# Performance work log

Hardware: AMD Instinct MI355X
Metric: run time of the kernel (lower is better)

Reference implementation:

```python
import jax, jax.numpy as jnp
import numpy as np

HIDDEN = 256
HEADS = 8
HEAD_DIM = HIDDEN // HEADS
NUM_RBF = 32
CUTOFF = 8.0
K_PTS = 4096   # total points (32 molecules x 128)
N_ATOMS = 2048 # total atoms  (32 molecules x 64)
B_MOL = 32


def setup_inputs() -> dict:
    key = jax.random.key(0)
    ks = jax.random.split(key, 12)
    s = 0.02
    return {
        "h_point": jax.random.normal(ks[0], (K_PTS, HIDDEN), jnp.float32),
        "h_atom": jax.random.normal(ks[1], (N_ATOMS, HIDDEN), jnp.float32),
        "pos_point": jax.random.uniform(ks[2], (K_PTS, 3), jnp.float32) * 10.0,
        "pos_atom": jax.random.uniform(ks[3], (N_ATOMS, 3), jnp.float32) * 10.0,
        "Wq": jax.random.normal(ks[4], (HIDDEN, HIDDEN), jnp.float32) * s,
        "bq": jnp.zeros((HIDDEN,), jnp.float32),
        "Wk": jax.random.normal(ks[5], (HIDDEN, HIDDEN), jnp.float32) * s,
        "bk": jnp.zeros((HIDDEN,), jnp.float32),
        "Wv": jax.random.normal(ks[6], (HIDDEN, HIDDEN), jnp.float32) * s,
        "bv": jnp.zeros((HIDDEN,), jnp.float32),
        "Wo": jax.random.normal(ks[7], (HIDDEN, HIDDEN), jnp.float32) * s,
        "bo": jnp.zeros((HIDDEN,), jnp.float32),
        "W_rbf": jax.random.normal(ks[8], (NUM_RBF, HEADS), jnp.float32) * 0.1,
        "b_rbf": jnp.zeros((HEADS,), jnp.float32),
        "centers": jnp.linspace(0.0, CUTOFF, NUM_RBF, dtype=jnp.float32),
        "gamma": jnp.ones((HIDDEN,), jnp.float32),
        "beta": jnp.zeros((HIDDEN,), jnp.float32),
        "point_batch": jnp.repeat(jnp.arange(B_MOL), K_PTS // B_MOL),
        "atom_batch": jnp.repeat(jnp.arange(B_MOL), N_ATOMS // B_MOL),
    }


def reference(h_point, h_atom, pos_point, pos_atom,
              Wq, bq, Wk, bk, Wv, bv, Wo, bo,
              W_rbf, b_rbf, centers, gamma, beta,
              point_batch, atom_batch):
    H, D = HEADS, HEAD_DIM
    Kp = h_point.shape[0]
    Na = h_atom.shape[0]
    scale = D ** -0.5
    width = (CUTOFF / NUM_RBF) ** 2

    q = (h_point @ Wq + bq).reshape(Kp, H, D)
    k = (h_atom @ Wk + bk).reshape(Na, H, D)
    v = (h_atom @ Wv + bv).reshape(Na, H, D)

    # pairwise distances [Kp, Na]
    d2 = jnp.sum((pos_point[:, None, :] - pos_atom[None, :, :]) ** 2, axis=-1)
    dist = jnp.sqrt(jnp.maximum(d2, 0.0))

    # RBF distance bias -> [H, Kp, Na]
    rbf = jnp.exp(-((dist[..., None] - centers) ** 2) / width)  # [Kp, Na, NUM_RBF]
    bias = (rbf @ W_rbf + b_rbf).transpose(2, 0, 1)

    scores = jnp.einsum('khd,nhd->hkn', q, k) * scale + bias
    # ragged structure: point j only attends to atoms in the same molecule
    mask = point_batch[:, None] == atom_batch[None, :]  # [Kp, Na]
    scores = jnp.where(mask[None], scores, -1e30)
    attn = jax.nn.softmax(scores, axis=-1)

    agg = jnp.einsum('hkn,nhd->khd', attn, v).reshape(Kp, H * D)
    agg = agg @ Wo + bo

    x = h_point + agg
    mean = jnp.mean(x, axis=-1, keepdims=True)
    var = jnp.mean((x - mean) ** 2, axis=-1, keepdims=True)
    return (x - mean) * jax.lax.rsqrt(var + 1e-5) * gamma + beta
```

## Files before the change

### kernel.cpp

```cpp
#include <hip/hip_runtime.h>
#include <hip/hip_bf16.h>

#define HIDDEN 256
#define HEADS 8
#define HEAD_DIM 32
#define NUM_RBF 32
#define K_PTS 4096
#define N_ATOMS 2048
#define B_MOL 32
#define ATOMS_PER_MOL (N_ATOMS / B_MOL)

typedef __attribute__((ext_vector_type(8))) short bf16x8;
typedef __attribute__((ext_vector_type(4))) float f32x4;

__global__ __launch_bounds__(256) void prepW_kernel(
    const float* __restrict__ Wq, const float* __restrict__ Wk,
    const float* __restrict__ Wv, const float* __restrict__ Wo,
    __hip_bfloat16* __restrict__ WqT, __hip_bfloat16* __restrict__ WkT,
    __hip_bfloat16* __restrict__ WvT, __hip_bfloat16* __restrict__ WoT) {
    __shared__ float tile[32][33];
    const int t = blockIdx.x, tid = threadIdx.x;
    const int matId = t >> 6, tileId = t & 63;
    const int tr = (tileId >> 3) * 32, tc = (tileId & 7) * 32;
    const float* __restrict__ Ws = (matId == 0) ? Wq : (matId == 1) ? Wk : (matId == 2) ? Wv : Wo;
    __hip_bfloat16* __restrict__ Wd = (matId == 0) ? WqT : (matId == 1) ? WkT : (matId == 2) ? WvT : WoT;

    const int r = tid >> 3, cq = (tid & 7) * 4;
    const float4 in = *(const float4*)&Ws[(size_t)(tr + r) * HIDDEN + tc + cq];
    tile[r][cq + 0] = in.x; tile[r][cq + 1] = in.y;
    tile[r][cq + 2] = in.z; tile[r][cq + 3] = in.w;
    __syncthreads();
    __hip_bfloat16 o[4];
    o[0] = __float2bfloat16(tile[cq + 0][r]);
    o[1] = __float2bfloat16(tile[cq + 1][r]);
    o[2] = __float2bfloat16(tile[cq + 2][r]);
    o[3] = __float2bfloat16(tile[cq + 3][r]);
    *(uint2*)(Wd + (size_t)(tc + r) * HIDDEN + tr + cq) = *(const uint2*)o;
}

__device__ __forceinline__ bf16x8 cvt8(const float* p) {
    const float4 lo = *(const float4*)p;
    const float4 hi = *(const float4*)(p + 4);
    __hip_bfloat16 t[8];
    t[0] = __float2bfloat16(lo.x); t[1] = __float2bfloat16(lo.y);
    t[2] = __float2bfloat16(lo.z); t[3] = __float2bfloat16(lo.w);
    t[4] = __float2bfloat16(hi.x); t[5] = __float2bfloat16(hi.y);
    t[6] = __float2bfloat16(hi.z); t[7] = __float2bfloat16(hi.w);
    return *(const bf16x8*)t;
}

__global__ __launch_bounds__(256) void qkv2_kernel(
    const float* __restrict__ hp, const float* __restrict__ ha,
    const __hip_bfloat16* __restrict__ WqT, const float* __restrict__ bq, float* __restrict__ q_ws,
    const __hip_bfloat16* __restrict__ WkT, const float* __restrict__ bk, float* __restrict__ k_ws,
    const __hip_bfloat16* __restrict__ WvT, const float* __restrict__ bv, float* __restrict__ v_ws) {
    const bool isQ = (blockIdx.x < 256);
    const float* __restrict__ A = isQ ? hp : ha;
    const __hip_bfloat16* __restrict__ W0T = isQ ? WqT : WkT;
    const float* __restrict__ b0 = isQ ? bq : bk;
    float* __restrict__ C0 = isQ ? q_ws : k_ws;
    const int r0 = (isQ ? blockIdx.x : blockIdx.x - 256) * 16;

    const int wave = threadIdx.x >> 6, lane = threadIdx.x & 63;
    const int c0 = wave * 64;
    const int lrow = lane & 15, kgrp = lane >> 4;

    bf16x8 af[8];
    const float* Arow = A + (size_t)(r0 + lrow) * HIDDEN + kgrp * 8;
#pragma unroll
    for (int ks = 0; ks < 8; ++ks)
        af[ks] = cvt8(Arow + ks * 32);

    f32x4 acc0[4], acc1[4];
#pragma unroll
    for (int cc = 0; cc < 4; ++cc) {
        acc0[cc] = (f32x4){0.f, 0.f, 0.f, 0.f};
        acc1[cc] = (f32x4){0.f, 0.f, 0.f, 0.f};
    }

#pragma unroll
    for (int cc = 0; cc < 4; ++cc) {
        const short* W0r = (const short*)W0T + (size_t)(c0 + cc * 16 + lrow) * HIDDEN + kgrp * 8;
#pragma unroll
        for (int ks = 0; ks < 8; ++ks)
            acc0[cc] = __builtin_amdgcn_mfma_f32_16x16x32_bf16(
                af[ks], *(const bf16x8*)(W0r + ks * 32), acc0[cc], 0, 0, 0);
        if (!isQ) {
            const short* W1r = (const short*)WvT + (size_t)(c0 + cc * 16 + lrow) * HIDDEN + kgrp * 8;
#pragma unroll
            for (int ks = 0; ks < 8; ++ks)
                acc1[cc] = __builtin_amdgcn_mfma_f32_16x16x32_bf16(
                    af[ks], *(const bf16x8*)(W1r + ks * 32), acc1[cc], 0, 0, 0);
        }
    }

    const int colb = lane & 15;
    const int rowb = (lane >> 4) * 4;
#pragma unroll
    for (int cc = 0; cc < 4; ++cc) {
        const int cgl = c0 + cc * 16 + colb;
        const float bias0 = b0[cgl];
#pragma unroll
        for (int rg = 0; rg < 4; ++rg)
            C0[(size_t)(r0 + rowb + rg) * HIDDEN + cgl] = acc0[cc][rg] + bias0;
        if (!isQ) {
            const float bias1 = bv[cgl];
#pragma unroll
            for (int rg = 0; rg < 4; ++rg)
                v_ws[(size_t)(r0 + rowb + rg) * HIDDEN + cgl] = acc1[cc][rg] + bias1;
        }
    }
}

#define AGG_PAD (HIDDEN + 16)
#define X_PAD (HIDDEN + 4)

__global__ __launch_bounds__(256) void attn_oln_kernel(
    const float* __restrict__ q, const float* __restrict__ kmat,
    const float* __restrict__ vmat,
    const float* __restrict__ pos_point, const float* __restrict__ pos_atom,
    const float* __restrict__ W_rbf, const float* __restrict__ b_rbf,
    const float* __restrict__ centers,
    const int* __restrict__ point_batch, const int* __restrict__ atom_batch,
    const __hip_bfloat16* __restrict__ WoT, const float* __restrict__ bo,
    const float* __restrict__ h_point,
    const float* __restrict__ gamma, const float* __restrict__ beta,
    float* __restrict__ out) {
    __shared__ float q_lds[8][HIDDEN];
    __shared__ float wrbf_lds[NUM_RBF][HEADS];
    __shared__ float cent_lds[NUM_RBF];
    __shared__ float brbf_lds[HEADS];
    __shared__ float w_lds[4][2][HEADS][72];
    __shared__ __hip_bfloat16 agg_lds[8][AGG_PAD];
    __shared__ float x_lds[8][X_PAD];
    __shared__ float red_s[8][4];
    __shared__ float red_q[8][4];

    const int tid = threadIdx.x, wave = tid >> 6, lane = tid & 63;
    const int j0 = blockIdx.x * 8;

    {
        const float4* s4 = (const float4*)(q + (size_t)j0 * HIDDEN);
        float4* d4 = (float4*)&q_lds[0][0];
        d4[tid] = s4[tid];
        d4[tid + 256] = s4[tid + 256];
    }
    if (tid < NUM_RBF * HEADS) ((float*)wrbf_lds)[tid] = W_rbf[tid];
    if (tid < NUM_RBF) cent_lds[tid] = centers[tid];
    if (tid < HEADS) brbf_lds[tid] = b_rbf[tid];
    __syncthreads();

    const int jA = j0 + wave * 2, jB = jA + 1;
    const int m = point_batch[jA];
    const int n = m * ATOMS_PER_MOL + lane;
    const bool valid = (atom_batch[n] == m);

    const float ax = pos_atom[n * 3 + 0], ay = pos_atom[n * 3 + 1], az = pos_atom[n * 3 + 2];
    const float dxA = pos_point[jA * 3 + 0] - ax;
    const float dyA = pos_point[jA * 3 + 1] - ay;
    const float dzA = pos_point[jA * 3 + 2] - az;
    const float dxB = pos_point[jB * 3 + 0] - ax;
    const float dyB = pos_point[jB * 3 + 1] - ay;
    const float dzB = pos_point[jB * 3 + 2] - az;
    const float distA = sqrtf(fmaxf(dxA * dxA + dyA * dyA + dzA * dzA, 0.0f));
    const float distB = sqrtf(fmaxf(dxB * dxB + dyB * dyB + dzB * dzB, 0.0f));

    float biasA[HEADS], biasB[HEADS];
#pragma unroll
    for (int h = 0; h < HEADS; ++h) { biasA[h] = brbf_lds[h]; biasB[h] = brbf_lds[h]; }
#pragma unroll
    for (int r = 0; r < NUM_RBF; ++r) {
        const float c = cent_lds[r];
        const float ddA = distA - c, ddB = distB - c;
        const float eA = __expf(-16.0f * ddA * ddA);
        const float eB = __expf(-16.0f * ddB * ddB);
#pragma unroll
        for (int h = 0; h < HEADS; ++h) {
            const float wr = wrbf_lds[r][h];
            biasA[h] += eA * wr;
            biasB[h] += eB * wr;
        }
    }

    const float scale = 0.17677669529663687f;
    const float* krow = kmat + (size_t)n * HIDDEN;

#pragma unroll
    for (int h = 0; h < HEADS; ++h) {
        const float4* k4 = (const float4*)(krow + h * HEAD_DIM);
        const float4* qA4 = (const float4*)(&q_lds[wave * 2 + 0][h * HEAD_DIM]);
        const float4* qB4 = (const float4*)(&q_lds[wave * 2 + 1][h * HEAD_DIM]);
        float dotA = 0.f, dotB = 0.f;
#pragma unroll
        for (int i = 0; i < HEAD_DIM / 4; ++i) {
            const float4 kv = k4[i];
            const float4 qa = qA4[i];
            const float4 qb = qB4[i];
            dotA += kv.x * qa.x + kv.y * qa.y + kv.z * qa.z + kv.w * qa.w;
            dotB += kv.x * qb.x + kv.y * qb.y + kv.z * qb.z + kv.w * qb.w;
        }
        float sA = valid ? (dotA * scale + biasA[h]) : -1e30f;
        float sB = valid ? (dotB * scale + biasB[h]) : -1e30f;

        float mA = sA, mB = sB;
#pragma unroll
        for (int off = 32; off > 0; off >>= 1) {
            mA = fmaxf(mA, __shfl_xor(mA, off));
            mB = fmaxf(mB, __shfl_xor(mB, off));
        }
        const float eA = __expf(sA - mA);
        const float eB = __expf(sB - mB);
        float ssA = eA, ssB = eB;
#pragma unroll
        for (int off = 32; off > 0; off >>= 1) {
            ssA += __shfl_xor(ssA, off);
            ssB += __shfl_xor(ssB, off);
        }
        w_lds[wave][0][h][lane] = eA / ssA;
        w_lds[wave][1][h][lane] = eB / ssB;
    }

    const int c4 = lane * 4;
    const int hh = lane >> 3;
    {
        const float* wA = &w_lds[wave][0][hh][0];
        const float* wB = &w_lds[wave][1][hh][0];
        const float* vbase = vmat + (size_t)(m * ATOMS_PER_MOL) * HIDDEN + c4;
        float4 accA = {0.f, 0.f, 0.f, 0.f};
        float4 accB = {0.f, 0.f, 0.f, 0.f};
#pragma unroll
        for (int a4 = 0; a4 < ATOMS_PER_MOL / 4; ++a4) {
            const float4 wa = *(const float4*)&wA[a4 * 4];
            const float4 wb = *(const float4*)&wB[a4 * 4];
            const float4 v0 = *(const float4*)(vbase + (size_t)(a4 * 4 + 0) * HIDDEN);
            const float4 v1 = *(const float4*)(vbase + (size_t)(a4 * 4 + 1) * HIDDEN);
            const float4 v2 = *(const float4*)(vbase + (size_t)(a4 * 4 + 2) * HIDDEN);
            const float4 v3 = *(const float4*)(vbase + (size_t)(a4 * 4 + 3) * HIDDEN);
            accA.x += wa.x * v0.x + wa.y * v1.x + wa.z * v2.x + wa.w * v3.x;
            accA.y += wa.x * v0.y + wa.y * v1.y + wa.z * v2.y + wa.w * v3.y;
            accA.z += wa.x * v0.z + wa.y * v1.z + wa.z * v2.z + wa.w * v3.z;
            accA.w += wa.x * v0.w + wa.y * v1.w + wa.z * v2.w + wa.w * v3.w;
            accB.x += wb.x * v0.x + wb.y * v1.x + wb.z * v2.x + wb.w * v3.x;
            accB.y += wb.x * v0.y + wb.y * v1.y + wb.z * v2.y + wb.w * v3.y;
            accB.z += wb.x * v0.z + wb.y * v1.z + wb.z * v2.z + wb.w * v3.z;
            accB.w += wb.x * v0.w + wb.y * v1.w + wb.z * v2.w + wb.w * v3.w;
        }
        __hip_bfloat16 oA[4], oB[4];
        oA[0] = __float2bfloat16(accA.x); oA[1] = __float2bfloat16(accA.y);
        oA[2] = __float2bfloat16(accA.z); oA[3] = __float2bfloat16(accA.w);
        oB[0] = __float2bfloat16(accB.x); oB[1] = __float2bfloat16(accB.y);
        oB[2] = __float2bfloat16(accB.z); oB[3] = __float2bfloat16(accB.w);
        *(uint2*)(&agg_lds[wave * 2 + 0][c4]) = *(const uint2*)oA;
        *(uint2*)(&agg_lds[wave * 2 + 1][c4]) = *(const uint2*)oB;
    }
    __syncthreads();

    const int c0 = wave * 64;
    const int lrow = lane & 15, kgrp = lane >> 4;
    bf16x8 af[8];
    const bf16x8 zf = {0, 0, 0, 0, 0, 0, 0, 0};
#pragma unroll
    for (int ks = 0; ks < 8; ++ks)
        af[ks] = (lrow < 8) ? *(const bf16x8*)(&agg_lds[lrow & 7][kgrp * 8 + ks * 32]) : zf;

    f32x4 acc[4];
#pragma unroll
    for (int cc = 0; cc < 4; ++cc) acc[cc] = (f32x4){0.f, 0.f, 0.f, 0.f};
#pragma unroll
    for (int cc = 0; cc < 4; ++cc) {
        const short* Wr = (const short*)WoT + (size_t)(c0 + cc * 16 + lrow) * HIDDEN + kgrp * 8;
#pragma unroll
        for (int ks = 0; ks < 8; ++ks)
            acc[cc] = __builtin_amdgcn_mfma_f32_16x16x32_bf16(
                af[ks], *(const bf16x8*)(Wr + ks * 32), acc[cc], 0, 0, 0);
    }

    const int colb = lane & 15;
    const int rowb = (lane >> 4) * 4;
#pragma unroll
    for (int cc = 0; cc < 4; ++cc) {
        const int cgl = c0 + cc * 16 + colb;
        const float bias = bo[cgl];
#pragma unroll
        for (int rg = 0; rg < 4; ++rg) {
            const int rl = rowb + rg;
            if (rl < 8)
                x_lds[rl][cgl] = acc[cc][rg] + bias + h_point[(size_t)(j0 + rl) * HIDDEN + cgl];
        }
    }
    __syncthreads();

    const int c = tid;
    const int ln = c & 63, wv = c >> 6;
    float xv[8];
#pragma unroll
    for (int r = 0; r < 8; ++r) {
        xv[r] = x_lds[r][c];
        float s = xv[r], qq = xv[r] * xv[r];
#pragma unroll
        for (int off = 32; off > 0; off >>= 1) {
            s += __shfl_xor(s, off);
            qq += __shfl_xor(qq, off);
        }
        if (ln == 0) { red_s[r][wv] = s; red_q[r][wv] = qq; }
    }
    __syncthreads();

    const float gc = gamma[c], bc = beta[c];
#pragma unroll
    for (int r = 0; r < 8; ++r) {
        const float mean = (red_s[r][0] + red_s[r][1] + red_s[r][2] + red_s[r][3]) * (1.0f / HIDDEN);
        const float ex2  = (red_q[r][0] + red_q[r][1] + red_q[r][2] + red_q[r][3]) * (1.0f / HIDDEN);
        const float var = ex2 - mean * mean;
        out[(size_t)(j0 + r) * HIDDEN + c] = (xv[r] - mean) * rsqrtf(var + 1e-5f) * gc + bc;
    }
}

extern "C" void kernel_launch(void* const* d_in, const int* in_sizes, int n_in,
                              void* d_out, int out_size, void* d_ws, size_t ws_size,
                              hipStream_t stream) {
    const float* h_point   = (const float*)d_in[0];
    const float* h_atom    = (const float*)d_in[1];
    const float* pos_point = (const float*)d_in[2];
    const float* pos_atom  = (const float*)d_in[3];
    const float* Wq        = (const float*)d_in[4];
    const float* bq        = (const float*)d_in[5];
    const float* Wk        = (const float*)d_in[6];
    const float* bk        = (const float*)d_in[7];
    const float* Wv        = (const float*)d_in[8];
    const float* bv        = (const float*)d_in[9];
    const float* Wo        = (const float*)d_in[10];
    const float* bo        = (const float*)d_in[11];
    const float* W_rbf     = (const float*)d_in[12];
    const float* b_rbf     = (const float*)d_in[13];
    const float* centers   = (const float*)d_in[14];
    const float* gamma     = (const float*)d_in[15];
    const float* beta      = (const float*)d_in[16];
    const int*   point_batch = (const int*)d_in[17];
    const int*   atom_batch  = (const int*)d_in[18];
    float* out = (float*)d_out;

    float* q_ws = (float*)d_ws;
    float* k_ws = q_ws + (size_t)K_PTS * HIDDEN;
    float* v_ws = k_ws + (size_t)N_ATOMS * HIDDEN;
    __hip_bfloat16* WqT = (__hip_bfloat16*)(v_ws + (size_t)N_ATOMS * HIDDEN);
    __hip_bfloat16* WkT = WqT + HIDDEN * HIDDEN;
    __hip_bfloat16* WvT = WkT + HIDDEN * HIDDEN;
    __hip_bfloat16* WoT = WvT + HIDDEN * HIDDEN;

    prepW_kernel<<<256, 256, 0, stream>>>(Wq, Wk, Wv, Wo, WqT, WkT, WvT, WoT);

    qkv2_kernel<<<384, 256, 0, stream>>>(h_point, h_atom,
                                         WqT, bq, q_ws,
                                         WkT, bk, k_ws,
                                         WvT, bv, v_ws);

    attn_oln_kernel<<<K_PTS / 8, 256, 0, stream>>>(q_ws, k_ws, v_ws,
                                                   pos_point, pos_atom,
                                                   W_rbf, b_rbf, centers,
                                                   point_batch, atom_batch,
                                                   WoT, bo, h_point, gamma, beta,
                                                   out);
}
```

Before: 146.7 us.

## Store K/V as bf16 and split attention work across waves by head

The Q/K/V projection kernel now writes K and V as bf16 instead of fp32, which halves the traffic for the attention kernel's K/V reads. The attention kernel is reorganized so each block handles 4 points instead of 8. Each wave now owns 2 heads across all 4 points rather than 2 points across all heads, which cuts per-thread RBF and exp work and lets K rows be reused across points. The grid doubles to 1024 blocks for better occupancy, at the cost of scalar 2-byte V loads and reduced precision for K/V.

```diff
diff --git a/kernel.cpp b/kernel.cpp
--- a/kernel.cpp
+++ b/kernel.cpp
@@ -52,13 +52,12 @@
 __global__ __launch_bounds__(256) void qkv2_kernel(
     const float* __restrict__ hp, const float* __restrict__ ha,
     const __hip_bfloat16* __restrict__ WqT, const float* __restrict__ bq, float* __restrict__ q_ws,
-    const __hip_bfloat16* __restrict__ WkT, const float* __restrict__ bk, float* __restrict__ k_ws,
-    const __hip_bfloat16* __restrict__ WvT, const float* __restrict__ bv, float* __restrict__ v_ws) {
+    const __hip_bfloat16* __restrict__ WkT, const float* __restrict__ bk, __hip_bfloat16* __restrict__ k_bf,
+    const __hip_bfloat16* __restrict__ WvT, const float* __restrict__ bv, __hip_bfloat16* __restrict__ v_bf) {
     const bool isQ = (blockIdx.x < 256);
     const float* __restrict__ A = isQ ? hp : ha;
     const __hip_bfloat16* __restrict__ W0T = isQ ? WqT : WkT;
     const float* __restrict__ b0 = isQ ? bq : bk;
-    float* __restrict__ C0 = isQ ? q_ws : k_ws;
     const int r0 = (isQ ? blockIdx.x : blockIdx.x - 256) * 16;
 
     const int wave = threadIdx.x >> 6, lane = threadIdx.x & 63;
@@ -100,24 +99,32 @@
     for (int cc = 0; cc < 4; ++cc) {
         const int cgl = c0 + cc * 16 + colb;
         const float bias0 = b0[cgl];
-#pragma unroll
-        for (int rg = 0; rg < 4; ++rg)
-            C0[(size_t)(r0 + rowb + rg) * HIDDEN + cgl] = acc0[cc][rg] + bias0;
-        if (!isQ) {
+        if (isQ) {
+#pragma unroll
+            for (int rg = 0; rg < 4; ++rg)
+                q_ws[(size_t)(r0 + rowb + rg) * HIDDEN + cgl] = acc0[cc][rg] + bias0;
+        } else {
             const float bias1 = bv[cgl];
 #pragma unroll
-            for (int rg = 0; rg < 4; ++rg)
-                v_ws[(size_t)(r0 + rowb + rg) * HIDDEN + cgl] = acc1[cc][rg] + bias1;
-        }
-    }
-}
-
+            for (int rg = 0; rg < 4; ++rg) {
+                k_bf[(size_t)(r0 + rowb + rg) * HIDDEN + cgl] = __float2bfloat16(acc0[cc][rg] + bias0);
+                v_bf[(size_t)(r0 + rowb + rg) * HIDDEN + cgl] = __float2bfloat16(acc1[cc][rg] + bias1);
+            }
+        }
+    }
+}
+
+#define W_PAD 72
 #define AGG_PAD (HIDDEN + 16)
-#define X_PAD (HIDDEN + 4)
-
-__global__ __launch_bounds__(256) void attn_oln_kernel(
-    const float* __restrict__ q, const float* __restrict__ kmat,
-    const float* __restrict__ vmat,
+
+__device__ __forceinline__ void unpack2(unsigned u, float& lo, float& hi) {
+    lo = __uint_as_float(u << 16);
+    hi = __uint_as_float(u & 0xffff0000u);
+}
+
+__global__ __launch_bounds__(256) void attn_oln4_kernel(
+    const float* __restrict__ q, const __hip_bfloat16* __restrict__ kmat,
+    const __hip_bfloat16* __restrict__ vmat,
     const float* __restrict__ pos_point, const float* __restrict__ pos_atom,
     const float* __restrict__ W_rbf, const float* __restrict__ b_rbf,
     const float* __restrict__ centers,
@@ -126,132 +133,131 @@
     const float* __restrict__ h_point,
     const float* __restrict__ gamma, const float* __restrict__ beta,
     float* __restrict__ out) {
-    __shared__ float q_lds[8][HIDDEN];
+    __shared__ float q_lds[4][260];
     __shared__ float wrbf_lds[NUM_RBF][HEADS];
     __shared__ float cent_lds[NUM_RBF];
     __shared__ float brbf_lds[HEADS];
-    __shared__ float w_lds[4][2][HEADS][72];
-    __shared__ __hip_bfloat16 agg_lds[8][AGG_PAD];
-    __shared__ float x_lds[8][X_PAD];
-    __shared__ float red_s[8][4];
-    __shared__ float red_q[8][4];
+    __shared__ float p_lds[4][2][4][W_PAD];
+    __shared__ __hip_bfloat16 agg_lds[4][AGG_PAD];
+    __shared__ float x_lds[4][260];
+    __shared__ float red_s[4][4];
+    __shared__ float red_q[4][4];
 
     const int tid = threadIdx.x, wave = tid >> 6, lane = tid & 63;
-    const int j0 = blockIdx.x * 8;
+    const int j0 = blockIdx.x * 4;
 
     {
-        const float4* s4 = (const float4*)(q + (size_t)j0 * HIDDEN);
-        float4* d4 = (float4*)&q_lds[0][0];
-        d4[tid] = s4[tid];
-        d4[tid + 256] = s4[tid + 256];
-    }
-    if (tid < NUM_RBF * HEADS) ((float*)wrbf_lds)[tid] = W_rbf[tid];
+        const int row = tid >> 6, c4 = (tid & 63) * 4;
+        *(float4*)&q_lds[row][c4] = *(const float4*)(q + (size_t)(j0 + row) * HIDDEN + c4);
+    }
+    ((float*)wrbf_lds)[tid & 255] = W_rbf[tid & 255];
     if (tid < NUM_RBF) cent_lds[tid] = centers[tid];
     if (tid < HEADS) brbf_lds[tid] = b_rbf[tid];
     __syncthreads();
 
-    const int jA = j0 + wave * 2, jB = jA + 1;
-    const int m = point_batch[jA];
+    const int m = point_batch[j0];
     const int n = m * ATOMS_PER_MOL + lane;
     const bool valid = (atom_batch[n] == m);
+    const int h0 = wave * 2;
 
     const float ax = pos_atom[n * 3 + 0], ay = pos_atom[n * 3 + 1], az = pos_atom[n * 3 + 2];
-    const float dxA = pos_point[jA * 3 + 0] - ax;
-    const float dyA = pos_point[jA * 3 + 1] - ay;
-    const float dzA = pos_point[jA * 3 + 2] - az;
-    const float dxB = pos_point[jB * 3 + 0] - ax;
-    const float dyB = pos_point[jB * 3 + 1] - ay;
-    const float dzB = pos_point[jB * 3 + 2] - az;
-    const float distA = sqrtf(fmaxf(dxA * dxA + dyA * dyA + dzA * dzA, 0.0f));
-    const float distB = sqrtf(fmaxf(dxB * dxB + dyB * dyB + dzB * dzB, 0.0f));
-
-    float biasA[HEADS], biasB[HEADS];
-#pragma unroll
-    for (int h = 0; h < HEADS; ++h) { biasA[h] = brbf_lds[h]; biasB[h] = brbf_lds[h]; }
+    float dist[4];
+#pragma unroll
+    for (int p = 0; p < 4; ++p) {
+        const float dx = pos_point[(j0 + p) * 3 + 0] - ax;
+        const float dy = pos_point[(j0 + p) * 3 + 1] - ay;
+        const float dz = pos_point[(j0 + p) * 3 + 2] - az;
+        dist[p] = sqrtf(fmaxf(dx * dx + dy * dy + dz * dz, 0.0f));
+    }
+
+    float bias[4][2];
+#pragma unroll
+    for (int p = 0; p < 4; ++p) {
+        bias[p][0] = brbf_lds[h0];
+        bias[p][1] = brbf_lds[h0 + 1];
+    }
 #pragma unroll
     for (int r = 0; r < NUM_RBF; ++r) {
-        const float c = cent_lds[r];
-        const float ddA = distA - c, ddB = distB - c;
-        const float eA = __expf(-16.0f * ddA * ddA);
-        const float eB = __expf(-16.0f * ddB * ddB);
-#pragma unroll
-        for (int h = 0; h < HEADS; ++h) {
-            const float wr = wrbf_lds[r][h];
-            biasA[h] += eA * wr;
-            biasB[h] += eB * wr;
+        const float cr = cent_lds[r];
+        const float w0 = wrbf_lds[r][h0], w1 = wrbf_lds[r][h0 + 1];
+#pragma unroll
+        for (int p = 0; p < 4; ++p) {
+            const float dd = dist[p] - cr;
+            const float e = __expf(-16.0f * dd * dd);
+            bias[p][0] += e * w0;
+            bias[p][1] += e * w1;
         }
     }
 
     const float scale = 0.17677669529663687f;
-    const float* krow = kmat + (size_t)n * HIDDEN;
-
-#pragma unroll
-    for (int h = 0; h < HEADS; ++h) {
-        const float4* k4 = (const float4*)(krow + h * HEAD_DIM);
-        const float4* qA4 = (const float4*)(&q_lds[wave * 2 + 0][h * HEAD_DIM]);
-        const float4* qB4 = (const float4*)(&q_lds[wave * 2 + 1][h * HEAD_DIM]);
-        float dotA = 0.f, dotB = 0.f;
-#pragma unroll
-        for (int i = 0; i < HEAD_DIM / 4; ++i) {
-            const float4 kv = k4[i];
-            const float4 qa = qA4[i];
-            const float4 qb = qB4[i];
-            dotA += kv.x * qa.x + kv.y * qa.y + kv.z * qa.z + kv.w * qa.w;
-            dotB += kv.x * qb.x + kv.y * qb.y + kv.z * qb.z + kv.w * qb.w;
-        }
-        float sA = valid ? (dotA * scale + biasA[h]) : -1e30f;
-        float sB = valid ? (dotB * scale + biasB[h]) : -1e30f;
-
-        float mA = sA, mB = sB;
-#pragma unroll
-        for (int off = 32; off > 0; off >>= 1) {
-            mA = fmaxf(mA, __shfl_xor(mA, off));
-            mB = fmaxf(mB, __shfl_xor(mB, off));
-        }
-        const float eA = __expf(sA - mA);
-        const float eB = __expf(sB - mB);
-        float ssA = eA, ssB = eB;
-#pragma unroll
-        for (int off = 32; off > 0; off >>= 1) {
-            ssA += __shfl_xor(ssA, off);
-            ssB += __shfl_xor(ssB, off);
-        }
-        w_lds[wave][0][h][lane] = eA / ssA;
-        w_lds[wave][1][h][lane] = eB / ssB;
-    }
-
-    const int c4 = lane * 4;
-    const int hh = lane >> 3;
+
+#pragma unroll
+    for (int hl = 0; hl < 2; ++hl) {
+        const unsigned* kr = (const unsigned*)((const unsigned short*)kmat +
+                             (size_t)n * HIDDEN + (h0 + hl) * HEAD_DIM);
+        float kf[32];
+#pragma unroll
+        for (int i = 0; i < 16; ++i)
+            unpack2(kr[i], kf[2 * i], kf[2 * i + 1]);
+
+        float dot[4] = {0.f, 0.f, 0.f, 0.f};
+#pragma unroll
+        for (int i = 0; i < 8; ++i) {
+            const int qo = (h0 + hl) * HEAD_DIM + i * 4;
+            const float4 q0 = *(const float4*)&q_lds[0][qo];
+            const float4 q1 = *(const float4*)&q_lds[1][qo];
+            const float4 q2 = *(const float4*)&q_lds[2][qo];
+            const float4 q3 = *(const float4*)&q_lds[3][qo];
+            dot[0] += q0.x * kf[4*i] + q0.y * kf[4*i+1] + q0.z * kf[4*i+2] + q0.w * kf[4*i+3];
+            dot[1] += q1.x * kf[4*i] + q1.y * kf[4*i+1] + q1.z * kf[4*i+2] + q1.w * kf[4*i+3];
+            dot[2] += q2.x * kf[4*i] + q2.y * kf[4*i+1] + q2.z * kf[4*i+2] + q2.w * kf[4*i+3];
+            dot[3] += q3.x * kf[4*i] + q3.y * kf[4*i+1] + q3.z * kf[4*i+2] + q3.w * kf[4*i+3];
+        }
+#pragma unroll
+        for (int p = 0; p < 4; ++p) {
+            float score = valid ? (dot[p] * scale + bias[p][hl]) : -1e30f;
+            float mx = score;
+#pragma unroll
+            for (int off = 32; off > 0; off >>= 1)
+                mx = fmaxf(mx, __shfl_xor(mx, off));
+            const float e = __expf(score - mx);
+            float ss = e;
+#pragma unroll
+            for (int off = 32; off > 0; off >>= 1)
+                ss += __shfl_xor(ss, off);
+            p_lds[wave][hl][p][lane] = e / ss;
+        }
+    }
+
     {
-        const float* wA = &w_lds[wave][0][hh][0];
-        const float* wB = &w_lds[wave][1][hh][0];
-        const float* vbase = vmat + (size_t)(m * ATOMS_PER_MOL) * HIDDEN + c4;
-        float4 accA = {0.f, 0.f, 0.f, 0.f};
-        float4 accB = {0.f, 0.f, 0.f, 0.f};
-#pragma unroll
-        for (int a4 = 0; a4 < ATOMS_PER_MOL / 4; ++a4) {
-            const float4 wa = *(const float4*)&wA[a4 * 4];
-            const float4 wb = *(const float4*)&wB[a4 * 4];
-            const float4 v0 = *(const float4*)(vbase + (size_t)(a4 * 4 + 0) * HIDDEN);
-            const float4 v1 = *(const float4*)(vbase + (size_t)(a4 * 4 + 1) * HIDDEN);
-            const float4 v2 = *(const float4*)(vbase + (size_t)(a4 * 4 + 2) * HIDDEN);
-            const float4 v3 = *(const float4*)(vbase + (size_t)(a4 * 4 + 3) * HIDDEN);
-            accA.x += wa.x * v0.x + wa.y * v1.x + wa.z * v2.x + wa.w * v3.x;
-            accA.y += wa.x * v0.y + wa.y * v1.y + wa.z * v2.y + wa.w * v3.y;
-            accA.z += wa.x * v0.z + wa.y * v1.z + wa.z * v2.z + wa.w * v3.z;
-            accA.w += wa.x * v0.w + wa.y * v1.w + wa.z * v2.w + wa.w * v3.w;
-            accB.x += wb.x * v0.x + wb.y * v1.x + wb.z * v2.x + wb.w * v3.x;
-            accB.y += wb.x * v0.y + wb.y * v1.y + wb.z * v2.y + wb.w * v3.y;
-            accB.z += wb.x * v0.z + wb.y * v1.z + wb.z * v2.z + wb.w * v3.z;
-            accB.w += wb.x * v0.w + wb.y * v1.w + wb.z * v2.w + wb.w * v3.w;
-        }
-        __hip_bfloat16 oA[4], oB[4];
-        oA[0] = __float2bfloat16(accA.x); oA[1] = __float2bfloat16(accA.y);
-        oA[2] = __float2bfloat16(accA.z); oA[3] = __float2bfloat16(accA.w);
-        oB[0] = __float2bfloat16(accB.x); oB[1] = __float2bfloat16(accB.y);
-        oB[2] = __float2bfloat16(accB.z); oB[3] = __float2bfloat16(accB.w);
-        *(uint2*)(&agg_lds[wave * 2 + 0][c4]) = *(const uint2*)oA;
-        *(uint2*)(&agg_lds[wave * 2 + 1][c4]) = *(const uint2*)oB;
+        const int c = tid;
+        const int hl2 = (lane >> 5) & 1;
+        const unsigned short* vbase = (const unsigned short*)vmat +
+                                      (size_t)(m * ATOMS_PER_MOL) * HIDDEN + c;
+        float acc[4] = {0.f, 0.f, 0.f, 0.f};
+#pragma unroll
+        for (int ag = 0; ag < ATOMS_PER_MOL / 4; ++ag) {
+            const float4 p0 = *(const float4*)&p_lds[wave][hl2][0][ag * 4];
+            const float4 p1 = *(const float4*)&p_lds[wave][hl2][1][ag * 4];
+            const float4 p2 = *(const float4*)&p_lds[wave][hl2][2][ag * 4];
+            const float4 p3 = *(const float4*)&p_lds[wave][hl2][3][ag * 4];
+            const float* pp0 = (const float*)&p0;
+            const float* pp1 = (const float*)&p1;
+            const float* pp2 = (const float*)&p2;
+            const float* pp3 = (const float*)&p3;
+#pragma unroll
+            for (int i = 0; i < 4; ++i) {
+                const int a = ag * 4 + i;
+                const float v = __uint_as_float(((unsigned)vbase[(size_t)a * HIDDEN]) << 16);
+                acc[0] += pp0[i] * v;
+                acc[1] += pp1[i] * v;
+                acc[2] += pp2[i] * v;
+                acc[3] += pp3[i] * v;
+            }
+        }
+#pragma unroll
+        for (int p = 0; p < 4; ++p)
+            agg_lds[p][c] = __float2bfloat16(acc[p]);
     }
     __syncthreads();
 
@@ -261,7 +267,7 @@
     const bf16x8 zf = {0, 0, 0, 0, 0, 0, 0, 0};
 #pragma unroll
     for (int ks = 0; ks < 8; ++ks)
-        af[ks] = (lrow < 8) ? *(const bf16x8*)(&agg_lds[lrow & 7][kgrp * 8 + ks * 32]) : zf;
+        af[ks] = (lrow < 4) ? *(const bf16x8*)(&agg_lds[lrow & 3][kgrp * 8 + ks * 32]) : zf;
 
     f32x4 acc[4];
 #pragma unroll
@@ -280,21 +286,21 @@
 #pragma unroll
     for (int cc = 0; cc < 4; ++cc) {
         const int cgl = c0 + cc * 16 + colb;
-        const float bias = bo[cgl];
+        const float bias_o = bo[cgl];
 #pragma unroll
         for (int rg = 0; rg < 4; ++rg) {
             const int rl = rowb + rg;
-            if (rl < 8)
-                x_lds[rl][cgl] = acc[cc][rg] + bias + h_point[(size_t)(j0 + rl) * HIDDEN + cgl];
+            if (rl < 4)
+                x_lds[rl][cgl] = acc[cc][rg] + bias_o + h_point[(size_t)(j0 + rl) * HIDDEN + cgl];
         }
     }
     __syncthreads();
 
     const int c = tid;
     const int ln = c & 63, wv = c >> 6;
-    float xv[8];
-#pragma unroll
-    for (int r = 0; r < 8; ++r) {
+    float xv[4];
+#pragma unroll
+    for (int r = 0; r < 4; ++r) {
         xv[r] = x_lds[r][c];
         float s = xv[r], qq = xv[r] * xv[r];
 #pragma unroll
@@ -308,7 +314,7 @@
 
     const float gc = gamma[c], bc = beta[c];
 #pragma unroll
-    for (int r = 0; r < 8; ++r) {
+    for (int r = 0; r < 4; ++r) {
         const float mean = (red_s[r][0] + red_s[r][1] + red_s[r][2] + red_s[r][3]) * (1.0f / HIDDEN);
         const float ex2  = (red_q[r][0] + red_q[r][1] + red_q[r][2] + red_q[r][3]) * (1.0f / HIDDEN);
         const float var = ex2 - mean * mean;
@@ -341,9 +347,9 @@
     float* out = (float*)d_out;
 
     float* q_ws = (float*)d_ws;
-    float* k_ws = q_ws + (size_t)K_PTS * HIDDEN;
-    float* v_ws = k_ws + (size_t)N_ATOMS * HIDDEN;
-    __hip_bfloat16* WqT = (__hip_bfloat16*)(v_ws + (size_t)N_ATOMS * HIDDEN);
+    __hip_bfloat16* k_bf = (__hip_bfloat16*)(q_ws + (size_t)K_PTS * HIDDEN);
+    __hip_bfloat16* v_bf = k_bf + (size_t)N_ATOMS * HIDDEN;
+    __hip_bfloat16* WqT = v_bf + (size_t)N_ATOMS * HIDDEN;
     __hip_bfloat16* WkT = WqT + HIDDEN * HIDDEN;
     __hip_bfloat16* WvT = WkT + HIDDEN * HIDDEN;
     __hip_bfloat16* WoT = WvT + HIDDEN * HIDDEN;
@@ -352,13 +358,13 @@
 
     qkv2_kernel<<<384, 256, 0, stream>>>(h_point, h_atom,
                                          WqT, bq, q_ws,
-                                         WkT, bk, k_ws,
-                                         WvT, bv, v_ws);
-
-    attn_oln_kernel<<<K_PTS / 8, 256, 0, stream>>>(q_ws, k_ws, v_ws,
-                                                   pos_point, pos_atom,
-                                                   W_rbf, b_rbf, centers,
-                                                   point_batch, atom_batch,
-                                                   WoT, bo, h_point, gamma, beta,
-                                                   out);
-}
+                                         WkT, bk, k_bf,
+                                         WvT, bv, v_bf);
+
+    attn_oln4_kernel<<<K_PTS / 4, 256, 0, stream>>>(q_ws, k_bf, v_bf,
+                                                    pos_point, pos_atom,
+                                                    W_rbf, b_rbf, centers,
+                                                    point_batch, atom_batch,
+                                                    WoT, bo, h_point, gamma, beta,
+                                                    out);
+}
```

After: 180.8 us. 23.2% more time.

## Compute attention scores and PV product with bf16 MFMA, store Q/K/V in bf16

Applied to the files above, without the earlier changes.

The QKV projection kernel now writes Q and K as bf16 and V transposed as bf16. The attention kernel swaps the scalar fp32 dot products and the weighted V sum for 16x16x32 bf16 MFMA instructions. The RBF bias is staged in LDS per head and atom, and the softmax runs on MFMA accumulator fragments using 16-lane shuffles. This cuts global traffic for Q/K/V and moves the attention arithmetic onto matrix cores, at the cost of lower precision on scores and probabilities and a strided transposed V store.

```diff
diff --git a/kernel.cpp b/kernel.cpp
--- a/kernel.cpp
+++ b/kernel.cpp
@@ -49,16 +49,15 @@
     return *(const bf16x8*)t;
 }
 
-__global__ __launch_bounds__(256) void qkv2_kernel(
+__global__ __launch_bounds__(256) void qkv3_kernel(
     const float* __restrict__ hp, const float* __restrict__ ha,
-    const __hip_bfloat16* __restrict__ WqT, const float* __restrict__ bq, float* __restrict__ q_ws,
-    const __hip_bfloat16* __restrict__ WkT, const float* __restrict__ bk, float* __restrict__ k_ws,
-    const __hip_bfloat16* __restrict__ WvT, const float* __restrict__ bv, float* __restrict__ v_ws) {
+    const __hip_bfloat16* __restrict__ WqT, const float* __restrict__ bq, __hip_bfloat16* __restrict__ qb,
+    const __hip_bfloat16* __restrict__ WkT, const float* __restrict__ bk, __hip_bfloat16* __restrict__ kb,
+    const __hip_bfloat16* __restrict__ WvT, const float* __restrict__ bv, __hip_bfloat16* __restrict__ vt) {
     const bool isQ = (blockIdx.x < 256);
     const float* __restrict__ A = isQ ? hp : ha;
     const __hip_bfloat16* __restrict__ W0T = isQ ? WqT : WkT;
     const float* __restrict__ b0 = isQ ? bq : bk;
-    float* __restrict__ C0 = isQ ? q_ws : k_ws;
     const int r0 = (isQ ? blockIdx.x : blockIdx.x - 256) * 16;
 
     const int wave = threadIdx.x >> 6, lane = threadIdx.x & 63;
@@ -100,24 +99,26 @@
     for (int cc = 0; cc < 4; ++cc) {
         const int cgl = c0 + cc * 16 + colb;
         const float bias0 = b0[cgl];
-#pragma unroll
-        for (int rg = 0; rg < 4; ++rg)
-            C0[(size_t)(r0 + rowb + rg) * HIDDEN + cgl] = acc0[cc][rg] + bias0;
-        if (!isQ) {
+        if (isQ) {
+#pragma unroll
+            for (int rg = 0; rg < 4; ++rg)
+                qb[(size_t)(r0 + rowb + rg) * HIDDEN + cgl] = __float2bfloat16(acc0[cc][rg] + bias0);
+        } else {
             const float bias1 = bv[cgl];
 #pragma unroll
-            for (int rg = 0; rg < 4; ++rg)
-                v_ws[(size_t)(r0 + rowb + rg) * HIDDEN + cgl] = acc1[cc][rg] + bias1;
+            for (int rg = 0; rg < 4; ++rg) {
+                kb[(size_t)(r0 + rowb + rg) * HIDDEN + cgl] = __float2bfloat16(acc0[cc][rg] + bias0);
+                vt[(size_t)cgl * N_ATOMS + (r0 + rowb + rg)] = __float2bfloat16(acc1[cc][rg] + bias1);
+            }
         }
     }
 }
 
 #define AGG_PAD (HIDDEN + 16)
-#define X_PAD (HIDDEN + 4)
-
-__global__ __launch_bounds__(256) void attn_oln_kernel(
-    const float* __restrict__ q, const float* __restrict__ kmat,
-    const float* __restrict__ vmat,
+
+__global__ __launch_bounds__(256) void attn_mfma_kernel(
+    const __hip_bfloat16* __restrict__ qb, const __hip_bfloat16* __restrict__ kb,
+    const __hip_bfloat16* __restrict__ vt,
     const float* __restrict__ pos_point, const float* __restrict__ pos_atom,
     const float* __restrict__ W_rbf, const float* __restrict__ b_rbf,
     const float* __restrict__ centers,
@@ -126,153 +127,159 @@
     const float* __restrict__ h_point,
     const float* __restrict__ gamma, const float* __restrict__ beta,
     float* __restrict__ out) {
-    __shared__ float q_lds[8][HIDDEN];
     __shared__ float wrbf_lds[NUM_RBF][HEADS];
     __shared__ float cent_lds[NUM_RBF];
     __shared__ float brbf_lds[HEADS];
-    __shared__ float w_lds[4][2][HEADS][72];
+    __shared__ float bias_lds[HEADS][ATOMS_PER_MOL + 1][8];
+    __shared__ __hip_bfloat16 p_lds[HEADS][8][72];
     __shared__ __hip_bfloat16 agg_lds[8][AGG_PAD];
-    __shared__ float x_lds[8][X_PAD];
+    __shared__ float x_lds[8][260];
     __shared__ float red_s[8][4];
     __shared__ float red_q[8][4];
 
     const int tid = threadIdx.x, wave = tid >> 6, lane = tid & 63;
     const int j0 = blockIdx.x * 8;
-
-    {
-        const float4* s4 = (const float4*)(q + (size_t)j0 * HIDDEN);
-        float4* d4 = (float4*)&q_lds[0][0];
-        d4[tid] = s4[tid];
-        d4[tid + 256] = s4[tid + 256];
-    }
-    if (tid < NUM_RBF * HEADS) ((float*)wrbf_lds)[tid] = W_rbf[tid];
+    const float scale = 0.17677669529663687f;
+
+    ((float*)wrbf_lds)[tid] = W_rbf[tid];
     if (tid < NUM_RBF) cent_lds[tid] = centers[tid];
     if (tid < HEADS) brbf_lds[tid] = b_rbf[tid];
-    __syncthreads();
-
-    const int jA = j0 + wave * 2, jB = jA + 1;
-    const int m = point_batch[jA];
-    const int n = m * ATOMS_PER_MOL + lane;
-    const bool valid = (atom_batch[n] == m);
-
-    const float ax = pos_atom[n * 3 + 0], ay = pos_atom[n * 3 + 1], az = pos_atom[n * 3 + 2];
-    const float dxA = pos_point[jA * 3 + 0] - ax;
-    const float dyA = pos_point[jA * 3 + 1] - ay;
-    const float dzA = pos_point[jA * 3 + 2] - az;
-    const float dxB = pos_point[jB * 3 + 0] - ax;
-    const float dyB = pos_point[jB * 3 + 1] - ay;
-    const float dzB = pos_point[jB * 3 + 2] - az;
-    const float distA = sqrtf(fmaxf(dxA * dxA + dyA * dyA + dzA * dzA, 0.0f));
-    const float distB = sqrtf(fmaxf(dxB * dxB + dyB * dyB + dzB * dzB, 0.0f));
-
-    float biasA[HEADS], biasB[HEADS];
-#pragma unroll
-    for (int h = 0; h < HEADS; ++h) { biasA[h] = brbf_lds[h]; biasB[h] = brbf_lds[h]; }
-#pragma unroll
-    for (int r = 0; r < NUM_RBF; ++r) {
-        const float c = cent_lds[r];
-        const float ddA = distA - c, ddB = distB - c;
-        const float eA = __expf(-16.0f * ddA * ddA);
-        const float eB = __expf(-16.0f * ddB * ddB);
+    if (tid < 64) {
+        bias_lds[tid >> 3][ATOMS_PER_MOL][tid & 7] = 0.0f;
+    }
+    __syncthreads();
+
+    const int m = point_batch[j0];
+    const int mbase = m * ATOMS_PER_MOL;
+
+    {
+        const int n = mbase + lane;
+        const bool valid = (atom_batch[n] == m);
+        const int jA = j0 + wave * 2, jB = jA + 1;
+
+        const float ax = pos_atom[n * 3 + 0], ay = pos_atom[n * 3 + 1], az = pos_atom[n * 3 + 2];
+        const float dxA = pos_point[jA * 3 + 0] - ax;
+        const float dyA = pos_point[jA * 3 + 1] - ay;
+        const float dzA = pos_point[jA * 3 + 2] - az;
+        const float dxB = pos_point[jB * 3 + 0] - ax;
+        const float dyB = pos_point[jB * 3 + 1] - ay;
+        const float dzB = pos_point[jB * 3 + 2] - az;
+        const float distA = sqrtf(fmaxf(dxA * dxA + dyA * dyA + dzA * dzA, 0.0f));
+        const float distB = sqrtf(fmaxf(dxB * dxB + dyB * dyB + dzB * dzB, 0.0f));
+
+        float biasA[HEADS], biasB[HEADS];
+#pragma unroll
+        for (int h = 0; h < HEADS; ++h) { biasA[h] = brbf_lds[h]; biasB[h] = brbf_lds[h]; }
+#pragma unroll
+        for (int r = 0; r < NUM_RBF; ++r) {
+            const float cr = cent_lds[r];
+            const float ddA = distA - cr, ddB = distB - cr;
+            const float eA = __expf(-16.0f * ddA * ddA);
+            const float eB = __expf(-16.0f * ddB * ddB);
+#pragma unroll
+            for (int h = 0; h < HEADS; ++h) {
+                const float wr = wrbf_lds[r][h];
+                biasA[h] += eA * wr;
+                biasB[h] += eB * wr;
+            }
+        }
 #pragma unroll
         for (int h = 0; h < HEADS; ++h) {
-            const float wr = wrbf_lds[r][h];
-            biasA[h] += eA * wr;
-            biasB[h] += eB * wr;
-        }
-    }
-
-    const float scale = 0.17677669529663687f;
-    const float* krow = kmat + (size_t)n * HIDDEN;
-
-#pragma unroll
-    for (int h = 0; h < HEADS; ++h) {
-        const float4* k4 = (const float4*)(krow + h * HEAD_DIM);
-        const float4* qA4 = (const float4*)(&q_lds[wave * 2 + 0][h * HEAD_DIM]);
-        const float4* qB4 = (const float4*)(&q_lds[wave * 2 + 1][h * HEAD_DIM]);
-        float dotA = 0.f, dotB = 0.f;
-#pragma unroll
-        for (int i = 0; i < HEAD_DIM / 4; ++i) {
-            const float4 kv = k4[i];
-            const float4 qa = qA4[i];
-            const float4 qb = qB4[i];
-            dotA += kv.x * qa.x + kv.y * qa.y + kv.z * qa.z + kv.w * qa.w;
-            dotB += kv.x * qb.x + kv.y * qb.y + kv.z * qb.z + kv.w * qb.w;
-        }
-        float sA = valid ? (dotA * scale + biasA[h]) : -1e30f;
-        float sB = valid ? (dotB * scale + biasB[h]) : -1e30f;
-
-        float mA = sA, mB = sB;
-#pragma unroll
-        for (int off = 32; off > 0; off >>= 1) {
-            mA = fmaxf(mA, __shfl_xor(mA, off));
-            mB = fmaxf(mB, __shfl_xor(mB, off));
-        }
-        const float eA = __expf(sA - mA);
-        const float eB = __expf(sB - mB);
-        float ssA = eA, ssB = eB;
-#pragma unroll
-        for (int off = 32; off > 0; off >>= 1) {
-            ssA += __shfl_xor(ssA, off);
-            ssB += __shfl_xor(ssB, off);
-        }
-        w_lds[wave][0][h][lane] = eA / ssA;
-        w_lds[wave][1][h][lane] = eB / ssB;
-    }
-
-    const int c4 = lane * 4;
-    const int hh = lane >> 3;
-    {
-        const float* wA = &w_lds[wave][0][hh][0];
-        const float* wB = &w_lds[wave][1][hh][0];
-        const float* vbase = vmat + (size_t)(m * ATOMS_PER_MOL) * HIDDEN + c4;
-        float4 accA = {0.f, 0.f, 0.f, 0.f};
-        float4 accB = {0.f, 0.f, 0.f, 0.f};
-#pragma unroll
-        for (int a4 = 0; a4 < ATOMS_PER_MOL / 4; ++a4) {
-            const float4 wa = *(const float4*)&wA[a4 * 4];
-            const float4 wb = *(const float4*)&wB[a4 * 4];
-            const float4 v0 = *(const float4*)(vbase + (size_t)(a4 * 4 + 0) * HIDDEN);
-            const float4 v1 = *(const float4*)(vbase + (size_t)(a4 * 4 + 1) * HIDDEN);
-            const float4 v2 = *(const float4*)(vbase + (size_t)(a4 * 4 + 2) * HIDDEN);
-            const float4 v3 = *(const float4*)(vbase + (size_t)(a4 * 4 + 3) * HIDDEN);
-            accA.x += wa.x * v0.x + wa.y * v1.x + wa.z * v2.x + wa.w * v3.x;
-            accA.y += wa.x * v0.y + wa.y * v1.y + wa.z * v2.y + wa.w * v3.y;
-            accA.z += wa.x * v0.z + wa.y * v1.z + wa.z * v2.z + wa.w * v3.z;
-            accA.w += wa.x * v0.w + wa.y * v1.w + wa.z * v2.w + wa.w * v3.w;
-            accB.x += wb.x * v0.x + wb.y * v1.x + wb.z * v2.x + wb.w * v3.x;
-            accB.y += wb.x * v0.y + wb.y * v1.y + wb.z * v2.y + wb.w * v3.y;
-            accB.z += wb.x * v0.z + wb.y * v1.z + wb.z * v2.z + wb.w * v3.z;
-            accB.w += wb.x * v0.w + wb.y * v1.w + wb.z * v2.w + wb.w * v3.w;
-        }
-        __hip_bfloat16 oA[4], oB[4];
-        oA[0] = __float2bfloat16(accA.x); oA[1] = __float2bfloat16(accA.y);
-        oA[2] = __float2bfloat16(accA.z); oA[3] = __float2bfloat16(accA.w);
-        oB[0] = __float2bfloat16(accB.x); oB[1] = __float2bfloat16(accB.y);
-        oB[2] = __float2bfloat16(accB.z); oB[3] = __float2bfloat16(accB.w);
-        *(uint2*)(&agg_lds[wave * 2 + 0][c4]) = *(const uint2*)oA;
-        *(uint2*)(&agg_lds[wave * 2 + 1][c4]) = *(const uint2*)oB;
+            bias_lds[h][lane][wave * 2 + 0] = valid ? biasA[h] : -1e30f;
+            bias_lds[h][lane][wave * 2 + 1] = valid ? biasB[h] : -1e30f;
+        }
+    }
+    __syncthreads();
+
+    const int c = lane & 15, kgrp = lane >> 4;
+    const int h0 = wave * 2;
+
+#pragma unroll
+    for (int hl = 0; hl < 2; ++hl) {
+        const int h = h0 + hl;
+
+        const bf16x8 aq = *(const bf16x8*)((const short*)qb +
+                          (size_t)(j0 + (c & 7)) * HIDDEN + h * HEAD_DIM + kgrp * 8);
+
+        f32x4 sacc[4];
+#pragma unroll
+        for (int t = 0; t < 4; ++t) {
+            const bf16x8 bk_ = *(const bf16x8*)((const short*)kb +
+                               (size_t)(mbase + c + 16 * t) * HIDDEN + h * HEAD_DIM + kgrp * 8);
+            sacc[t] = __builtin_amdgcn_mfma_f32_16x16x32_bf16(
+                aq, bk_, (f32x4){0.f, 0.f, 0.f, 0.f}, 0, 0, 0);
+        }
+
+        float s[4][4];
+#pragma unroll
+        for (int t = 0; t < 4; ++t) {
+            const f32x4 bv = *(const f32x4*)&bias_lds[h][c + 16 * t][kgrp * 4];
+#pragma unroll
+            for (int r = 0; r < 4; ++r)
+                s[t][r] = sacc[t][r] * scale + bv[r];
+        }
+#pragma unroll
+        for (int r = 0; r < 4; ++r) {
+            float mx = fmaxf(fmaxf(s[0][r], s[1][r]), fmaxf(s[2][r], s[3][r]));
+#pragma unroll
+            for (int off = 1; off <= 8; off <<= 1)
+                mx = fmaxf(mx, __shfl_xor(mx, off));
+            float e0 = __expf(s[0][r] - mx);
+            float e1 = __expf(s[1][r] - mx);
+            float e2 = __expf(s[2][r] - mx);
+            float e3 = __expf(s[3][r] - mx);
+            float ss = e0 + e1 + e2 + e3;
+#pragma unroll
+            for (int off = 1; off <= 8; off <<= 1)
+                ss += __shfl_xor(ss, off);
+            const float inv = 1.0f / ss;
+            if (kgrp < 2) {
+                const int pt = kgrp * 4 + r;
+                p_lds[h][pt][c + 16 * 0] = __float2bfloat16(e0 * inv);
+                p_lds[h][pt][c + 16 * 1] = __float2bfloat16(e1 * inv);
+                p_lds[h][pt][c + 16 * 2] = __float2bfloat16(e2 * inv);
+                p_lds[h][pt][c + 16 * 3] = __float2bfloat16(e3 * inv);
+            }
+        }
+
+#pragma unroll
+        for (int t2 = 0; t2 < 2; ++t2) {
+            f32x4 pacc = (f32x4){0.f, 0.f, 0.f, 0.f};
+#pragma unroll
+            for (int ks = 0; ks < 2; ++ks) {
+                const bf16x8 ap = *(const bf16x8*)&p_lds[h][c & 7][ks * 32 + kgrp * 8];
+                const bf16x8 bvv = *(const bf16x8*)((const short*)vt +
+                                   (size_t)(h * HEAD_DIM + t2 * 16 + c) * N_ATOMS +
+                                   mbase + ks * 32 + kgrp * 8);
+                pacc = __builtin_amdgcn_mfma_f32_16x16x32_bf16(ap, bvv, pacc, 0, 0, 0);
+            }
+            if (kgrp < 2) {
+#pragma unroll
+                for (int r = 0; r < 4; ++r)
+                    agg_lds[kgrp * 4 + r][h * HEAD_DIM + t2 * 16 + c] = __float2bfloat16(pacc[r]);
+            }
+        }
     }
     __syncthreads();
 
     const int c0 = wave * 64;
-    const int lrow = lane & 15, kgrp = lane >> 4;
+    const int lrow = lane & 15, kgrp2 = lane >> 4;
     bf16x8 af[8];
     const bf16x8 zf = {0, 0, 0, 0, 0, 0, 0, 0};
 #pragma unroll
     for (int ks = 0; ks < 8; ++ks)
-        af[ks] = (lrow < 8) ? *(const bf16x8*)(&agg_lds[lrow & 7][kgrp * 8 + ks * 32]) : zf;
-
-    f32x4 acc[4];
-#pragma unroll
-    for (int cc = 0; cc < 4; ++cc) acc[cc] = (f32x4){0.f, 0.f, 0.f, 0.f};
-#pragma unroll
-    for (int cc = 0; cc < 4; ++cc) {
-        const short* Wr = (const short*)WoT + (size_t)(c0 + cc * 16 + lrow) * HIDDEN + kgrp * 8;
+        af[ks] = (lrow < 8) ? *(const bf16x8*)(&agg_lds[lrow & 7][kgrp2 * 8 + ks * 32]) : zf;
+
+    f32x4 oacc[4];
+#pragma unroll
+    for (int cc = 0; cc < 4; ++cc) oacc[cc] = (f32x4){0.f, 0.f, 0.f, 0.f};
+#pragma unroll
+    for (int cc = 0; cc < 4; ++cc) {
+        const short* Wr = (const short*)WoT + (size_t)(c0 + cc * 16 + lrow) * HIDDEN + kgrp2 * 8;
 #pragma unroll
         for (int ks = 0; ks < 8; ++ks)
-            acc[cc] = __builtin_amdgcn_mfma_f32_16x16x32_bf16(
-                af[ks], *(const bf16x8*)(Wr + ks * 32), acc[cc], 0, 0, 0);
+            oacc[cc] = __builtin_amdgcn_mfma_f32_16x16x32_bf16(
+                af[ks], *(const bf16x8*)(Wr + ks * 32), oacc[cc], 0, 0, 0);
     }
 
     const int colb = lane & 15;
@@ -280,22 +287,22 @@
 #pragma unroll
     for (int cc = 0; cc < 4; ++cc) {
         const int cgl = c0 + cc * 16 + colb;
-        const float bias = bo[cgl];
+        const float bias_o = bo[cgl];
 #pragma unroll
         for (int rg = 0; rg < 4; ++rg) {
             const int rl = rowb + rg;
             if (rl < 8)
-                x_lds[rl][cgl] = acc[cc][rg] + bias + h_point[(size_t)(j0 + rl) * HIDDEN + cgl];
-        }
-    }
-    __syncthreads();
-
-    const int c = tid;
-    const int ln = c & 63, wv = c >> 6;
+                x_lds[rl][cgl] = oacc[cc][rg] + bias_o + h_point[(size_t)(j0 + rl) * HIDDEN + cgl];
+        }
+    }
+    __syncthreads();
+
+    const int cc2 = tid;
+    const int ln = cc2 & 63, wv = cc2 >> 6;
     float xv[8];
 #pragma unroll
     for (int r = 0; r < 8; ++r) {
-        xv[r] = x_lds[r][c];
+        xv[r] = x_lds[r][cc2];
         float s = xv[r], qq = xv[r] * xv[r];
 #pragma unroll
         for (int off = 32; off > 0; off >>= 1) {
@@ -306,13 +313,13 @@
     }
     __syncthreads();
 
-    const float gc = gamma[c], bc = beta[c];
+    const float gc = gamma[cc2], bc = beta[cc2];
 #pragma unroll
     for (int r = 0; r < 8; ++r) {
         const float mean = (red_s[r][0] + red_s[r][1] + red_s[r][2] + red_s[r][3]) * (1.0f / HIDDEN);
         const float ex2  = (red_q[r][0] + red_q[r][1] + red_q[r][2] + red_q[r][3]) * (1.0f / HIDDEN);
         const float var = ex2 - mean * mean;
-        out[(size_t)(j0 + r) * HIDDEN + c] = (xv[r] - mean) * rsqrtf(var + 1e-5f) * gc + bc;
+        out[(size_t)(j0 + r) * HIDDEN + cc2] = (xv[r] - mean) * rsqrtf(var + 1e-5f) * gc + bc;
     }
 }
 
@@ -340,25 +347,25 @@
     const int*   atom_batch  = (const int*)d_in[18];
     float* out = (float*)d_out;
 
-    float* q_ws = (float*)d_ws;
-    float* k_ws = q_ws + (size_t)K_PTS * HIDDEN;
-    float* v_ws = k_ws + (size_t)N_ATOMS * HIDDEN;
-    __hip_bfloat16* WqT = (__hip_bfloat16*)(v_ws + (size_t)N_ATOMS * HIDDEN);
+    __hip_bfloat16* qb = (__hip_bfloat16*)d_ws;
+    __hip_bfloat16* kb = qb + (size_t)K_PTS * HIDDEN;
+    __hip_bfloat16* vt = kb + (size_t)N_ATOMS * HIDDEN;
+    __hip_bfloat16* WqT = vt + (size_t)HIDDEN * N_ATOMS;
     __hip_bfloat16* WkT = WqT + HIDDEN * HIDDEN;
     __hip_bfloat16* WvT = WkT + HIDDEN * HIDDEN;
     __hip_bfloat16* WoT = WvT + HIDDEN * HIDDEN;
 
     prepW_kernel<<<256, 256, 0, stream>>>(Wq, Wk, Wv, Wo, WqT, WkT, WvT, WoT);
 
-    qkv2_kernel<<<384, 256, 0, stream>>>(h_point, h_atom,
-                                         WqT, bq, q_ws,
-                                         WkT, bk, k_ws,
-                                         WvT, bv, v_ws);
-
-    attn_oln_kernel<<<K_PTS / 8, 256, 0, stream>>>(q_ws, k_ws, v_ws,
-                                                   pos_point, pos_atom,
-                                                   W_rbf, b_rbf, centers,
-                                                   point_batch, atom_batch,
-                                                   WoT, bo, h_point, gamma, beta,
-                                                   out);
-}
+    qkv3_kernel<<<384, 256, 0, stream>>>(h_point, h_atom,
+                                         WqT, bq, qb,
+                                         WkT, bk, kb,
+                                         WvT, bv, vt);
+
+    attn_mfma_kernel<<<K_PTS / 8, 256, 0, stream>>>(qb, kb, vt,
+                                                    pos_point, pos_atom,
+                                                    W_rbf, b_rbf, centers,
+                                                    point_batch, atom_batch,
+                                                    WoT, bo, h_point, gamma, beta,
+                                                    out);
+}
```

New measurement: 137.1 us. 1.07x faster.
